# Performance work log

Hardware: AMD Instinct MI355X
Metric: run time of the kernel (lower is better)

## Reference

```python
import jax, jax.numpy as jnp
import numpy as np

N_NODES = 100000
N_EDGES = 1600000
N_GRAPHS = 1024
TIME_DIM = 64
HID = 32
HEADS = 4
NEG_SLOPE = 0.2


def _gat_layer(x, src, dst, W, a_src, a_dst, bias, heads, out_dim):
    # PyG GATConv: h = x @ W, per-head attention, segment softmax over incoming edges at dst.
    N = x.shape[0]
    h = (x @ W).reshape(N, heads, out_dim)                     # [N, H, D]
    alpha_src = jnp.sum(h * a_src, axis=-1)                    # [N, H]
    alpha_dst = jnp.sum(h * a_dst, axis=-1)                    # [N, H]
    e = alpha_src[src] + alpha_dst[dst]                        # [E, H]
    e = jnp.where(e > 0, e, NEG_SLOPE * e)                     # LeakyReLU(0.2)
    m = jax.ops.segment_max(e, dst, num_segments=N)            # [N, H]
    m = jnp.where(jnp.isfinite(m), m, 0.0)
    ex = jnp.exp(e - m[dst])                                   # [E, H]
    s = jax.ops.segment_sum(ex, dst, num_segments=N)           # [N, H]
    alpha = ex / (s[dst] + 1e-16)                              # [E, H]
    msg = h[src] * alpha[..., None]                            # [E, H, D]
    out = jax.ops.segment_sum(msg, dst, num_segments=N)        # [N, H, D]
    return out.reshape(N, heads * out_dim) + bias


def setup_inputs() -> dict:
    key = jax.random.key(0)
    ks = jax.random.split(key, 12)
    x = jax.random.normal(ks[0], (N_NODES, TIME_DIM), jnp.float32)
    edge_index = jax.random.randint(ks[1], (2, N_EDGES), 0, N_NODES, jnp.int32)
    batch = jnp.sort(jax.random.randint(ks[2], (N_NODES,), 0, N_GRAPHS, jnp.int32))
    s = 0.1
    params = {
        "W1": jax.random.normal(ks[3], (TIME_DIM, HEADS * HID), jnp.float32) * s,
        "a_src1": jax.random.normal(ks[4], (HEADS, HID), jnp.float32) * s,
        "a_dst1": jax.random.normal(ks[5], (HEADS, HID), jnp.float32) * s,
        "b1": jnp.zeros((HEADS * HID,), jnp.float32),
        "W2": jax.random.normal(ks[6], (HEADS * HID, HID), jnp.float32) * s,
        "a_src2": jax.random.normal(ks[7], (1, HID), jnp.float32) * s,
        "a_dst2": jax.random.normal(ks[8], (1, HID), jnp.float32) * s,
        "b2": jnp.zeros((HID,), jnp.float32),
        "Wc": jax.random.normal(ks[9], (HID, 1), jnp.float32) * s,
        "bc": jnp.zeros((1,), jnp.float32),
    }
    return dict(x=x, edge_index=edge_index, batch=batch, **params)


def reference(x, edge_index, batch, W1, a_src1, a_dst1, b1, W2, a_src2, a_dst2, b2, Wc, bc):
    N = x.shape[0]
    # PyG GATConv adds self-loops by default.
    loops = jnp.arange(N, dtype=edge_index.dtype)
    src = jnp.concatenate([edge_index[0], loops])
    dst = jnp.concatenate([edge_index[1], loops])

    h1 = jax.nn.relu(_gat_layer(x, src, dst, W1, a_src1, a_dst1, b1, HEADS, HID))
    h2 = jax.nn.relu(_gat_layer(h1, src, dst, W2, a_src2, a_dst2, b2, 1, HID))

    # global_mean_pool over batch ids
    sums = jax.ops.segment_sum(h2, batch, num_segments=N_GRAPHS)          # [G, HID]
    cnts = jax.ops.segment_sum(jnp.ones((N,), h2.dtype), batch, num_segments=N_GRAPHS)
    pooled = sums / jnp.maximum(cnts, 1.0)[:, None]

    return jax.nn.sigmoid(pooled @ Wc + bc)                               # [G, 1]
```

## Files before the change

### kernel.cpp

```cpp
#include <hip/hip_runtime.h>
#include <hip/hip_bf16.h>

#define BSH 7
#define MAXNB 800
#define STILE 4096
#define BCAP 4096

#if __has_builtin(__builtin_amdgcn_cvt_scalef32_pk_fp4_f32) && __has_builtin(__builtin_amdgcn_cvt_scalef32_pk_f32_fp4)
#define USE_FP4 1
#else
#define USE_FP4 0
#endif

__device__ inline float bf_lo(unsigned u) { return __uint_as_float(u << 16); }
__device__ inline float bf_hi(unsigned u) { return __uint_as_float(u & 0xffff0000u); }
__device__ inline unsigned bfpack(float x, float y) {
    unsigned lo = (unsigned)__bfloat16_as_ushort(__float2bfloat16(x));
    unsigned hi = ((unsigned)__bfloat16_as_ushort(__float2bfloat16(y))) << 16;
    return lo | hi;
}


__global__ __launch_bounds__(256) void k_bscatter(const int* __restrict__ ei, int E, int NB,
                                                  int* __restrict__ bcur, int* __restrict__ pairs) {
    __shared__ int lh[MAXNB];
    __shared__ int lbase[MAXNB];
    int t = threadIdx.x;
    int e0 = blockIdx.x * STILE;
    int e1 = min(E, e0 + STILE);
    for (int i = t; i < NB; i += 256) lh[i] = 0;
    __syncthreads();
    int myd[16];
    int q = 0;
    for (int e = e0 + t; e < e1; e += 256, q++) {
        int d = ei[E + e];
        myd[q] = d;
        atomicAdd(&lh[d >> BSH], 1);
    }
    __syncthreads();
    for (int i = t; i < NB; i += 256) {
        int c = lh[i];
        lbase[i] = c ? atomicAdd(&bcur[i], c) : 0;
    }
    __syncthreads();
    for (int i = t; i < NB; i += 256) lh[i] = 0;
    __syncthreads();
    q = 0;
    for (int e = e0 + t; e < e1; e += 256, q++) {
        int s = ei[e];
        int d = myd[q];
        int bk = d >> BSH;
        int off = atomicAdd(&lh[bk], 1);
        pairs[(size_t)bk * BCAP + lbase[bk] + off] = (s << BSH) | (d & ((1 << BSH) - 1));
    }
}

__global__ __launch_bounds__(256) void k_build(const int* __restrict__ pairs,
                                               const int* __restrict__ bcur, int N, int NB,
                                               int2* __restrict__ span, int* __restrict__ csr) {
    __shared__ int lcnt[128];
    __shared__ int loff[128];
    __shared__ int lcur[128];
    int b = blockIdx.x, t = threadIdx.x;
    int node0 = b << BSH;
    size_t base = (size_t)b * BCAP;
    int ne = bcur[b];
    if (t < 128) lcnt[t] = 0;
    __syncthreads();
    for (int i = t; i < ne; i += 256) atomicAdd(&lcnt[pairs[base + i] & 127], 1);
    __syncthreads();
    if (t < 128) loff[t] = lcnt[t];
    __syncthreads();
#pragma unroll
    for (int off = 1; off < 128; off <<= 1) {
        int v = (t < 128 && t >= off) ? loff[t - off] : 0;
        __syncthreads();
        if (t < 128) loff[t] += v;
        __syncthreads();
    }
    if (t < 128) {
        int excl = loff[t] - lcnt[t];
        int n = node0 + t;
        if (n < N) span[n] = make_int2((int)base + excl, (int)base + excl + lcnt[t]);
        lcur[t] = excl;
    }
    __syncthreads();
    for (int i = t; i < ne; i += 256) {
        int p = pairs[base + i];
        int pos = (int)base + atomicAdd(&lcur[p & 127], 1);
        csr[pos] = ((unsigned)p) >> BSH;
    }
}


__global__ __launch_bounds__(256) void k_gemm1(const float* __restrict__ x, const float* __restrict__ W1,
                                               const float* __restrict__ asw, const float* __restrict__ adw,
                                               unsigned* __restrict__ h8, float2* __restrict__ aP,
                                               float2* __restrict__ aDp, int N) {
    __shared__ float xt[64][36];
    int t = threadIdx.x;
    int n0 = blockIdx.x * 32;
    for (int i = t; i < 32 * 64; i += 256) {
        int r = i >> 6, k = i & 63;
        xt[k][r] = (n0 + r < N) ? x[(size_t)(n0 + r) * 64 + k] : 0.f;
    }
    __syncthreads();
    int cg = t & 31, rg = t >> 5;
    int c0 = cg * 4, r0 = rg * 4;
    int head = c0 >> 5;
    const float* Wp = W1 + c0;
    float acc[4][4];
#pragma unroll
    for (int r = 0; r < 4; r++)
#pragma unroll
        for (int c = 0; c < 4; c++) acc[r][c] = 0.f;
#pragma unroll 4
    for (int k = 0; k < 64; k++) {
        float4 wv = *(const float4*)(Wp + (size_t)k * 128);
        float4 xv = *(const float4*)&xt[k][r0];
        float xr;
        xr = xv.x; acc[0][0]=fmaf(xr,wv.x,acc[0][0]); acc[0][1]=fmaf(xr,wv.y,acc[0][1]); acc[0][2]=fmaf(xr,wv.z,acc[0][2]); acc[0][3]=fmaf(xr,wv.w,acc[0][3]);
        xr = xv.y; acc[1][0]=fmaf(xr,wv.x,acc[1][0]); acc[1][1]=fmaf(xr,wv.y,acc[1][1]); acc[1][2]=fmaf(xr,wv.z,acc[1][2]); acc[1][3]=fmaf(xr,wv.w,acc[1][3]);
        xr = xv.z; acc[2][0]=fmaf(xr,wv.x,acc[2][0]); acc[2][1]=fmaf(xr,wv.y,acc[2][1]); acc[2][2]=fmaf(xr,wv.z,acc[2][2]); acc[2][3]=fmaf(xr,wv.w,acc[2][3]);
        xr = xv.w; acc[3][0]=fmaf(xr,wv.x,acc[3][0]); acc[3][1]=fmaf(xr,wv.y,acc[3][1]); acc[3][2]=fmaf(xr,wv.z,acc[3][2]); acc[3][3]=fmaf(xr,wv.w,acc[3][3]);
    }
#if USE_FP4
#pragma unroll
    for (int r = 0; r < 4; r++) {
        int n = n0 + r0 + r;
        if (n < N) {
            unsigned u = __builtin_amdgcn_cvt_scalef32_pk_fp4_f32(0u, acc[r][0], acc[r][1], 1.0f, 0);
            u = __builtin_amdgcn_cvt_scalef32_pk_fp4_f32(u, acc[r][2], acc[r][3], 1.0f, 1);
            ((unsigned short*)h8)[(size_t)n * 32 + (c0 >> 2)] = (unsigned short)(u & 0xffffu);
        }
    }
#else
#pragma unroll
    for (int r = 0; r < 4; r++) {
        int n = n0 + r0 + r;
        if (n < N) {
            int u = __builtin_amdgcn_cvt_pk_fp8_f32(acc[r][0], acc[r][1], 0, false);
            u = __builtin_amdgcn_cvt_pk_fp8_f32(acc[r][2], acc[r][3], u, true);
            h8[(size_t)n * 32 + (c0 >> 2)] = (unsigned)u;
        }
    }
#endif
    float4 awv = *(const float4*)(asw + c0);
    float4 dwv = *(const float4*)(adw + c0);
#pragma unroll
    for (int r = 0; r < 4; r++) {
        float as = acc[r][0] * awv.x + acc[r][1] * awv.y + acc[r][2] * awv.z + acc[r][3] * awv.w;
        float ad = acc[r][0] * dwv.x + acc[r][1] * dwv.y + acc[r][2] * dwv.z + acc[r][3] * dwv.w;
#pragma unroll
        for (int m = 1; m < 8; m <<= 1) { as += __shfl_xor(as, m); ad += __shfl_xor(ad, m); }
        int n = n0 + r0 + r;
        if ((t & 7) == 0 && n < N) {
            aP[n * 4 + head]  = make_float2(__expf(as), __expf(0.2f * as));
            aDp[n * 4 + head] = make_float2(__expf(ad), __expf(0.2f * ad));
        }
    }
}


#if USE_FP4
__device__ inline void fp4fma(unsigned u, float w, float* a) {
    auto f0 = __builtin_amdgcn_cvt_scalef32_pk_f32_fp4(u, 1.0f, 0);
    auto f1 = __builtin_amdgcn_cvt_scalef32_pk_f32_fp4(u, 1.0f, 1);
    auto f2 = __builtin_amdgcn_cvt_scalef32_pk_f32_fp4(u, 1.0f, 2);
    auto f3 = __builtin_amdgcn_cvt_scalef32_pk_f32_fp4(u, 1.0f, 3);
    a[0] = fmaf(w, f0[0], a[0]); a[1] = fmaf(w, f0[1], a[1]);
    a[2] = fmaf(w, f1[0], a[2]); a[3] = fmaf(w, f1[1], a[3]);
    a[4] = fmaf(w, f2[0], a[4]); a[5] = fmaf(w, f2[1], a[5]);
    a[6] = fmaf(w, f3[0], a[6]); a[7] = fmaf(w, f3[1], a[7]);
}

__global__ __launch_bounds__(256) void k_gat1(const unsigned* __restrict__ h4,
                                              const float2* __restrict__ aP, const float2* __restrict__ aDp,
                                              const int2* __restrict__ span, const int* __restrict__ csr,
                                              const float* __restrict__ b1, unsigned* __restrict__ out, int N) {
    int t = threadIdx.x;
    int n = blockIdx.x * 4 + (t >> 6);
    if (n >= N) return;
    int lane = t & 63;
    int e4 = lane >> 4, c = lane & 15;
    int head = c >> 2;
    float2 dnp = aDp[n * 4 + head];
    float ec = dnp.x, ed = dnp.y;
    float2 psf = aP[n * 4 + head];
    float w_self = fmaxf(psf.x * ec, psf.y * ed);
    int2 sp = span[n];
    int beg = sp.x, end = sp.y;

    float a[8] = {0, 0, 0, 0, 0, 0, 0, 0};
    float s = 0.f;
    if (e4 == 0) {
        unsigned u = h4[(size_t)n * 16 + c];
        fp4fma(u, w_self, a);
        s = w_self;
    }
    int j = beg + e4;
    for (; j + 4 < end; j += 8) {
        int s0 = csr[j], s1 = csr[j + 4];
        float2 p0 = aP[s0 * 4 + head], p1 = aP[s1 * 4 + head];
        unsigned u0 = h4[(size_t)s0 * 16 + c];
        unsigned u1 = h4[(size_t)s1 * 16 + c];
        float w0 = fmaxf(p0.x * ec, p0.y * ed);
        float w1 = fmaxf(p1.x * ec, p1.y * ed);
        s += w0 + w1;
        fp4fma(u0, w0, a);
        fp4fma(u1, w1, a);
    }
    for (; j < end; j += 4) {
        int sj = csr[j];
        float2 p = aP[sj * 4 + head];
        unsigned u = h4[(size_t)sj * 16 + c];
        float w = fmaxf(p.x * ec, p.y * ed);
        s += w;
        fp4fma(u, w, a);
    }
#pragma unroll
    for (int off = 16; off < 64; off <<= 1) {
#pragma unroll
        for (int i = 0; i < 8; i++) a[i] += __shfl_xor(a[i], off);
        s += __shfl_xor(s, off);
    }
    if (e4 == 0) {
        float inv = 1.f / (s + 1e-16f);
        float4 ba = ((const float4*)b1)[c * 2];
        float4 bb = ((const float4*)b1)[c * 2 + 1];
        float o0 = fmaxf(fmaf(a[0], inv, ba.x), 0.f);
        float o1 = fmaxf(fmaf(a[1], inv, ba.y), 0.f);
        float o2 = fmaxf(fmaf(a[2], inv, ba.z), 0.f);
        float o3 = fmaxf(fmaf(a[3], inv, ba.w), 0.f);
        float o4 = fmaxf(fmaf(a[4], inv, bb.x), 0.f);
        float o5 = fmaxf(fmaf(a[5], inv, bb.y), 0.f);
        float o6 = fmaxf(fmaf(a[6], inv, bb.z), 0.f);
        float o7 = fmaxf(fmaf(a[7], inv, bb.w), 0.f);
        uint4 o;
        o.x = bfpack(o0, o1); o.y = bfpack(o2, o3);
        o.z = bfpack(o4, o5); o.w = bfpack(o6, o7);
        ((uint4*)out)[(size_t)n * 16 + c] = o;
    }
}
#else
__global__ __launch_bounds__(256) void k_gat1(const unsigned* __restrict__ h8,
                                              const float2* __restrict__ aP, const float2* __restrict__ aDp,
                                              const int2* __restrict__ span, const int* __restrict__ csr,
                                              const float* __restrict__ b1, unsigned* __restrict__ out, int N) {
    int t = threadIdx.x;
    int n = blockIdx.x * 4 + (t >> 6);
    if (n >= N) return;
    int lane = t & 63;
    int e2 = lane >> 5, c = lane & 31;
    int head = c >> 3;
    float2 dnp = aDp[n * 4 + head];
    float ec = dnp.x, ed = dnp.y;
    float2 psf = aP[n * 4 + head];
    float w_self = fmaxf(psf.x * ec, psf.y * ed);
    int2 sp = span[n];
    int beg = sp.x, end = sp.y;

    float a0 = 0.f, a1 = 0.f, a2 = 0.f, a3 = 0.f, s = 0.f;
    if (e2 == 0) {
        unsigned u = h8[(size_t)n * 32 + c];
        auto f01 = __builtin_amdgcn_cvt_pk_f32_fp8((int)u, false);
        auto f23 = __builtin_amdgcn_cvt_pk_f32_fp8((int)u, true);
        a0 = w_self * f01[0]; a1 = w_self * f01[1];
        a2 = w_self * f23[0]; a3 = w_self * f23[1];
        s = w_self;
    }
    int j = beg + e2;
    for (; j + 6 < end; j += 8) {
        int s0 = csr[j], s1 = csr[j + 2], s2 = csr[j + 4], s3 = csr[j + 6];
        float2 p0 = aP[s0 * 4 + head];
        float2 p1 = aP[s1 * 4 + head];
        float2 p2 = aP[s2 * 4 + head];
        float2 p3 = aP[s3 * 4 + head];
        unsigned u0 = h8[(size_t)s0 * 32 + c];
        unsigned u1 = h8[(size_t)s1 * 32 + c];
        unsigned u2 = h8[(size_t)s2 * 32 + c];
        unsigned u3 = h8[(size_t)s3 * 32 + c];
        float w0 = fmaxf(p0.x * ec, p0.y * ed);
        float w1 = fmaxf(p1.x * ec, p1.y * ed);
        float w2 = fmaxf(p2.x * ec, p2.y * ed);
        float w3 = fmaxf(p3.x * ec, p3.y * ed);
        s += w0 + w1 + w2 + w3;
        { auto f01 = __builtin_amdgcn_cvt_pk_f32_fp8((int)u0, false); auto f23 = __builtin_amdgcn_cvt_pk_f32_fp8((int)u0, true);
          a0 = fmaf(w0, f01[0], a0); a1 = fmaf(w0, f01[1], a1); a2 = fmaf(w0, f23[0], a2); a3 = fmaf(w0, f23[1], a3); }
        { auto f01 = __builtin_amdgcn_cvt_pk_f32_fp8((int)u1, false); auto f23 = __builtin_amdgcn_cvt_pk_f32_fp8((int)u1, true);
          a0 = fmaf(w1, f01[0], a0); a1 = fmaf(w1, f01[1], a1); a2 = fmaf(w1, f23[0], a2); a3 = fmaf(w1, f23[1], a3); }
        { auto f01 = __builtin_amdgcn_cvt_pk_f32_fp8((int)u2, false); auto f23 = __builtin_amdgcn_cvt_pk_f32_fp8((int)u2, true);
          a0 = fmaf(w2, f01[0], a0); a1 = fmaf(w2, f01[1], a1); a2 = fmaf(w2, f23[0], a2); a3 = fmaf(w2, f23[1], a3); }
        { auto f01 = __builtin_amdgcn_cvt_pk_f32_fp8((int)u3, false); auto f23 = __builtin_amdgcn_cvt_pk_f32_fp8((int)u3, true);
          a0 = fmaf(w3, f01[0], a0); a1 = fmaf(w3, f01[1], a1); a2 = fmaf(w3, f23[0], a2); a3 = fmaf(w3, f23[1], a3); }
    }
    for (; j < end; j += 2) {
        int sj = csr[j];
        float2 p = aP[sj * 4 + head];
        unsigned u = h8[(size_t)sj * 32 + c];
        float w = fmaxf(p.x * ec, p.y * ed);
        s += w;
        auto f01 = __builtin_amdgcn_cvt_pk_f32_fp8((int)u, false);
        auto f23 = __builtin_amdgcn_cvt_pk_f32_fp8((int)u, true);
        a0 = fmaf(w, f01[0], a0); a1 = fmaf(w, f01[1], a1);
        a2 = fmaf(w, f23[0], a2); a3 = fmaf(w, f23[1], a3);
    }
    a0 += __shfl_xor(a0, 32); a1 += __shfl_xor(a1, 32);
    a2 += __shfl_xor(a2, 32); a3 += __shfl_xor(a3, 32);
    s  += __shfl_xor(s, 32);
    if (e2 == 0) {
        float inv = 1.f / (s + 1e-16f);
        float4 b = ((const float4*)b1)[c];
        float o0 = fmaxf(fmaf(a0, inv, b.x), 0.f);
        float o1 = fmaxf(fmaf(a1, inv, b.y), 0.f);
        float o2 = fmaxf(fmaf(a2, inv, b.z), 0.f);
        float o3 = fmaxf(fmaf(a3, inv, b.w), 0.f);
        ((uint2*)out)[(size_t)n * 32 + c] = make_uint2(bfpack(o0, o1), bfpack(o2, o3));
    }
}
#endif


__global__ __launch_bounds__(256) void k_gemm2(const unsigned* __restrict__ h1b, const float* __restrict__ W2,
                                               const float* __restrict__ asw, const float* __restrict__ adw,
                                               unsigned short* __restrict__ h8, float2* __restrict__ aP,
                                               float2* __restrict__ aDp, int N) {
    __shared__ float xt[128][36];
    int t = threadIdx.x;
    int n0 = blockIdx.x * 32;
    for (int i = t; i < 32 * 64; i += 256) {
        int r = i >> 6, c = i & 63;
        unsigned u = (n0 + r < N) ? h1b[(size_t)(n0 + r) * 64 + c] : 0u;
        xt[2 * c][r]     = bf_lo(u);
        xt[2 * c + 1][r] = bf_hi(u);
    }
    __syncthreads();
    int col = t & 31, grp = t >> 5;
    const float* Wc = W2 + col;
    float acc[4] = {0, 0, 0, 0};
#pragma unroll 4
    for (int k = 0; k < 128; k++) {
        float w = Wc[k * 32];
        float4 xv = *(const float4*)&xt[k][grp * 4];
        acc[0] = fmaf(xv.x, w, acc[0]); acc[1] = fmaf(xv.y, w, acc[1]);
        acc[2] = fmaf(xv.z, w, acc[2]); acc[3] = fmaf(xv.w, w, acc[3]);
    }
    float aw = asw[col], dw = adw[col];
#pragma unroll
    for (int i = 0; i < 4; i++) {
        int n = n0 + grp * 4 + i;
        float other = __shfl_xor(acc[i], 1);
        if (((col & 1) == 0) && n < N) {
            int pk = __builtin_amdgcn_cvt_pk_fp8_f32(acc[i], other, 0, false);
            h8[(size_t)n * 16 + (col >> 1)] = (unsigned short)pk;
        }
        float as = acc[i] * aw, ad = acc[i] * dw;
#pragma unroll
        for (int mm = 16; mm >= 1; mm >>= 1) { as += __shfl_xor(as, mm); ad += __shfl_xor(ad, mm); }
        if (col == 0 && n < N) {
            aP[n]  = make_float2(__expf(as), __expf(0.2f * as));
            aDp[n] = make_float2(__expf(ad), __expf(0.2f * ad));
        }
    }
}


__global__ __launch_bounds__(256) void k_gat2(const unsigned* __restrict__ h8,
                                              const float2* __restrict__ aP, const float2* __restrict__ aDp,
                                              const int2* __restrict__ span, const int* __restrict__ csr,
                                              const float* __restrict__ b2, float* __restrict__ out, int N) {
    int t = threadIdx.x;
    int n = blockIdx.x * 4 + (t >> 6);
    if (n >= N) return;
    int lane = t & 63;
    int e8 = lane >> 3, c = lane & 7;
    float2 dnp = aDp[n];
    float ec = dnp.x, ed = dnp.y;
    float2 psf = aP[n];
    float w_self = fmaxf(psf.x * ec, psf.y * ed);
    int2 sp = span[n];
    int beg = sp.x, end = sp.y;

    float a0 = 0.f, a1 = 0.f, a2 = 0.f, a3 = 0.f, s = 0.f;
    if (e8 == 0) {
        unsigned u = h8[(size_t)n * 8 + c];
        auto f01 = __builtin_amdgcn_cvt_pk_f32_fp8((int)u, false);
        auto f23 = __builtin_amdgcn_cvt_pk_f32_fp8((int)u, true);
        a0 = w_self * f01[0]; a1 = w_self * f01[1];
        a2 = w_self * f23[0]; a3 = w_self * f23[1];
        s = w_self;
    }
    int j = beg + e8;
    for (; j + 24 < end; j += 32) {
        int s0 = csr[j], s1 = csr[j + 8], s2 = csr[j + 16], s3 = csr[j + 24];
        float2 p0 = aP[s0], p1 = aP[s1], p2 = aP[s2], p3 = aP[s3];
        unsigned u0 = h8[(size_t)s0 * 8 + c];
        unsigned u1 = h8[(size_t)s1 * 8 + c];
        unsigned u2 = h8[(size_t)s2 * 8 + c];
        unsigned u3 = h8[(size_t)s3 * 8 + c];
        float w0 = fmaxf(p0.x * ec, p0.y * ed);
        float w1 = fmaxf(p1.x * ec, p1.y * ed);
        float w2 = fmaxf(p2.x * ec, p2.y * ed);
        float w3 = fmaxf(p3.x * ec, p3.y * ed);
        s += w0 + w1 + w2 + w3;
        { auto f01 = __builtin_amdgcn_cvt_pk_f32_fp8((int)u0, false); auto f23 = __builtin_amdgcn_cvt_pk_f32_fp8((int)u0, true);
          a0 = fmaf(w0, f01[0], a0); a1 = fmaf(w0, f01[1], a1); a2 = fmaf(w0, f23[0], a2); a3 = fmaf(w0, f23[1], a3); }
        { auto f01 = __builtin_amdgcn_cvt_pk_f32_fp8((int)u1, false); auto f23 = __builtin_amdgcn_cvt_pk_f32_fp8((int)u1, true);
          a0 = fmaf(w1, f01[0], a0); a1 = fmaf(w1, f01[1], a1); a2 = fmaf(w1, f23[0], a2); a3 = fmaf(w1, f23[1], a3); }
        { auto f01 = __builtin_amdgcn_cvt_pk_f32_fp8((int)u2, false); auto f23 = __builtin_amdgcn_cvt_pk_f32_fp8((int)u2, true);
          a0 = fmaf(w2, f01[0], a0); a1 = fmaf(w2, f01[1], a1); a2 = fmaf(w2, f23[0], a2); a3 = fmaf(w2, f23[1], a3); }
        { auto f01 = __builtin_amdgcn_cvt_pk_f32_fp8((int)u3, false); auto f23 = __builtin_amdgcn_cvt_pk_f32_fp8((int)u3, true);
          a0 = fmaf(w3, f01[0], a0); a1 = fmaf(w3, f01[1], a1); a2 = fmaf(w3, f23[0], a2); a3 = fmaf(w3, f23[1], a3); }
    }
    for (; j < end; j += 8) {
        int sj = csr[j];
        float2 p = aP[sj];
        unsigned u = h8[(size_t)sj * 8 + c];
        float w = fmaxf(p.x * ec, p.y * ed);
        s += w;
        auto f01 = __builtin_amdgcn_cvt_pk_f32_fp8((int)u, false);
        auto f23 = __builtin_amdgcn_cvt_pk_f32_fp8((int)u, true);
        a0 = fmaf(w, f01[0], a0); a1 = fmaf(w, f01[1], a1);
        a2 = fmaf(w, f23[0], a2); a3 = fmaf(w, f23[1], a3);
    }
#pragma unroll
    for (int off = 8; off < 64; off <<= 1) {
        a0 += __shfl_xor(a0, off); a1 += __shfl_xor(a1, off);
        a2 += __shfl_xor(a2, off); a3 += __shfl_xor(a3, off);
        s  += __shfl_xor(s, off);
    }
    if (e8 == 0) {
        float inv = 1.f / (s + 1e-16f);
        float4 b = ((const float4*)b2)[c];
        float4 o;
        o.x = fmaxf(fmaf(a0, inv, b.x), 0.f);
        o.y = fmaxf(fmaf(a1, inv, b.y), 0.f);
        o.z = fmaxf(fmaf(a2, inv, b.z), 0.f);
        o.w = fmaxf(fmaf(a3, inv, b.w), 0.f);
        ((float4*)out)[(size_t)n * 8 + c] = o;
    }
}


__global__ void k_pool(const float* __restrict__ h2r, const int* __restrict__ batch, int N,
                       const float* __restrict__ Wc, const float* __restrict__ bc,
                       float* __restrict__ out) {
    int g = blockIdx.x;
    int t = threadIdx.x, d = t & 31, r = t >> 5;
    int lo = 0, hi = N;
    while (lo < hi) { int mid = (lo + hi) >> 1; if (batch[mid] < g) lo = mid + 1; else hi = mid; }
    int start = lo;
    hi = N;
    while (lo < hi) { int mid = (lo + hi) >> 1; if (batch[mid] < g + 1) lo = mid + 1; else hi = mid; }
    int end = lo;
    float sum = 0.f;
    for (int i = start + r; i < end; i += 2) sum += h2r[(size_t)i * 32 + d];
    sum += __shfl_xor(sum, 32);
    float cnt = (float)(end - start);
    float mean = sum / fmaxf(cnt, 1.f);
    float v = mean * Wc[d];
#pragma unroll
    for (int m = 16; m >= 1; m >>= 1) v += __shfl_xor(v, m);
    if (t == 0) out[g] = 1.f / (1.f + expf(-(v + bc[0])));
}


extern "C" void kernel_launch(void* const* d_in, const int* in_sizes, int n_in,
                              void* d_out, int out_size, void* d_ws, size_t ws_size,
                              hipStream_t stream) {
    const float* x    = (const float*)d_in[0];
    const int*   ei   = (const int*)d_in[1];
    const int*   batch= (const int*)d_in[2];
    const float* W1   = (const float*)d_in[3];
    const float* as1  = (const float*)d_in[4];
    const float* ad1  = (const float*)d_in[5];
    const float* b1   = (const float*)d_in[6];
    const float* W2   = (const float*)d_in[7];
    const float* as2  = (const float*)d_in[8];
    const float* ad2  = (const float*)d_in[9];
    const float* b2   = (const float*)d_in[10];
    const float* Wc   = (const float*)d_in[11];
    const float* bc   = (const float*)d_in[12];

    const int N = in_sizes[0] / 64;
    const int E = in_sizes[1] / 2;
    const int G = out_size;
    const int NB = (N + 127) >> BSH;

    size_t off = 0;
    char* base = (char*)d_ws;
    auto alloc = [&](size_t bytes) -> char* {
        char* p = base + off;
        off += (bytes + 255) & ~(size_t)255;
        return p;
    };
    int*      bcur  = (int*)alloc((size_t)NB * 4);
    int*      pairs = (int*)alloc((size_t)NB * BCAP * 4);
    int2*     span  = (int2*)alloc((size_t)N * 8);
    int*      csr   = (int*)alloc((size_t)NB * BCAP * 4);
    unsigned* h8_1  = (unsigned*)alloc((size_t)N * 128);
    unsigned* h1b   = (unsigned*)alloc((size_t)N * 64 * 4);
    float2*   aP1   = (float2*)alloc((size_t)N * 4 * 8);
    float2*   aDp1  = (float2*)alloc((size_t)N * 4 * 8);
    unsigned short* h8_2 = (unsigned short*)alloc((size_t)N * 32);
    float*    h2r   = (float*)alloc((size_t)N * 32 * 4);
    float2*   aP2   = (float2*)alloc((size_t)N * 8);
    float2*   aDp2  = (float2*)alloc((size_t)N * 8);
    (void)ws_size; (void)n_in;

    hipMemsetAsync(bcur, 0, (size_t)NB * 4, stream);
    k_bscatter<<<(E + STILE - 1) / STILE, 256, 0, stream>>>(ei, E, NB, bcur, pairs);
    k_build<<<NB, 256, 0, stream>>>(pairs, bcur, N, NB, span, csr);

    k_gemm1<<<(N + 31) / 32, 256, 0, stream>>>(x, W1, as1, ad1, h8_1, aP1, aDp1, N);
    k_gat1<<<(N + 3) / 4, 256, 0, stream>>>(h8_1, aP1, aDp1, span, csr, b1, h1b, N);

    k_gemm2<<<(N + 31) / 32, 256, 0, stream>>>(h1b, W2, as2, ad2, h8_2, aP2, aDp2, N);
    k_gat2<<<(N + 3) / 4, 256, 0, stream>>>((const unsigned*)h8_2, aP2, aDp2, span, csr, b2, h2r, N);

    k_pool<<<G, 64, 0, stream>>>(h2r, batch, N, Wc, bc, (float*)d_out);
}
```

Before: 237.2 us.

## Fuse scatter with gemm1, pack attention coefs to bf16, fp4 layer2, atomic pooling

Merges the edge bucket-scatter and the first projection GEMM into one launch, with blocks split by index, and removes the fp8 fallback path. The per-node source attention exponentials are packed as bf16 pairs instead of float2, which halves gather traffic in both GAT layers. Layer-2 features are stored as fp4, and the GAT2 epilogue atomically accumulates into per-graph pooled sums. This removes the h2 round trip and the pool reduction, but adds float-atomic contention and extra quantization error.

```diff
diff --git a/kernel.cpp b/kernel.cpp
--- a/kernel.cpp
+++ b/kernel.cpp
@@ -5,12 +5,6 @@
 #define MAXNB 800
 #define STILE 4096
 #define BCAP 4096
-
-#if __has_builtin(__builtin_amdgcn_cvt_scalef32_pk_fp4_f32) && __has_builtin(__builtin_amdgcn_cvt_scalef32_pk_f32_fp4)
-#define USE_FP4 1
-#else
-#define USE_FP4 0
-#endif
 
 __device__ inline float bf_lo(unsigned u) { return __uint_as_float(u << 16); }
 __device__ inline float bf_hi(unsigned u) { return __uint_as_float(u & 0xffff0000u); }
@@ -20,40 +14,109 @@
     return lo | hi;
 }
 
-
-__global__ __launch_bounds__(256) void k_bscatter(const int* __restrict__ ei, int E, int NB,
-                                                  int* __restrict__ bcur, int* __restrict__ pairs) {
-    __shared__ int lh[MAXNB];
-    __shared__ int lbase[MAXNB];
+__device__ inline void fp4fma(unsigned u, float w, float* a) {
+    auto f0 = __builtin_amdgcn_cvt_scalef32_pk_f32_fp4(u, 1.0f, 0);
+    auto f1 = __builtin_amdgcn_cvt_scalef32_pk_f32_fp4(u, 1.0f, 1);
+    auto f2 = __builtin_amdgcn_cvt_scalef32_pk_f32_fp4(u, 1.0f, 2);
+    auto f3 = __builtin_amdgcn_cvt_scalef32_pk_f32_fp4(u, 1.0f, 3);
+    a[0] = fmaf(w, f0[0], a[0]); a[1] = fmaf(w, f0[1], a[1]);
+    a[2] = fmaf(w, f1[0], a[2]); a[3] = fmaf(w, f1[1], a[3]);
+    a[4] = fmaf(w, f2[0], a[4]); a[5] = fmaf(w, f2[1], a[5]);
+    a[6] = fmaf(w, f3[0], a[6]); a[7] = fmaf(w, f3[1], a[7]);
+}
+
+
+__global__ __launch_bounds__(256) void k_front(const int* __restrict__ ei, int E, int NB,
+                                               int* __restrict__ bcur, int* __restrict__ pairs,
+                                               const float* __restrict__ x, const float* __restrict__ W1,
+                                               const float* __restrict__ asw, const float* __restrict__ adw,
+                                               unsigned* __restrict__ h4, unsigned* __restrict__ aPq,
+                                               float2* __restrict__ aDp, int N, int nbsc) {
+    __shared__ union USm {
+        struct { int lh[MAXNB]; int lbase[MAXNB]; } sc;
+        float xt[64][36];
+    } sm;
     int t = threadIdx.x;
-    int e0 = blockIdx.x * STILE;
-    int e1 = min(E, e0 + STILE);
-    for (int i = t; i < NB; i += 256) lh[i] = 0;
-    __syncthreads();
-    int myd[16];
-    int q = 0;
-    for (int e = e0 + t; e < e1; e += 256, q++) {
-        int d = ei[E + e];
-        myd[q] = d;
-        atomicAdd(&lh[d >> BSH], 1);
-    }
-    __syncthreads();
-    for (int i = t; i < NB; i += 256) {
-        int c = lh[i];
-        lbase[i] = c ? atomicAdd(&bcur[i], c) : 0;
-    }
-    __syncthreads();
-    for (int i = t; i < NB; i += 256) lh[i] = 0;
-    __syncthreads();
-    q = 0;
-    for (int e = e0 + t; e < e1; e += 256, q++) {
-        int s = ei[e];
-        int d = myd[q];
-        int bk = d >> BSH;
-        int off = atomicAdd(&lh[bk], 1);
-        pairs[(size_t)bk * BCAP + lbase[bk] + off] = (s << BSH) | (d & ((1 << BSH) - 1));
-    }
-}
+    if (blockIdx.x < nbsc) {
+        int e0 = blockIdx.x * STILE;
+        int e1 = min(E, e0 + STILE);
+        for (int i = t; i < NB; i += 256) sm.sc.lh[i] = 0;
+        __syncthreads();
+        int myd[16];
+        int q = 0;
+        for (int e = e0 + t; e < e1; e += 256, q++) {
+            int d = ei[E + e];
+            myd[q] = d;
+            atomicAdd(&sm.sc.lh[d >> BSH], 1);
+        }
+        __syncthreads();
+        for (int i = t; i < NB; i += 256) {
+            int c = sm.sc.lh[i];
+            sm.sc.lbase[i] = c ? atomicAdd(&bcur[i], c) : 0;
+        }
+        __syncthreads();
+        for (int i = t; i < NB; i += 256) sm.sc.lh[i] = 0;
+        __syncthreads();
+        q = 0;
+        for (int e = e0 + t; e < e1; e += 256, q++) {
+            int s = ei[e];
+            int d = myd[q];
+            int bk = d >> BSH;
+            int off = atomicAdd(&sm.sc.lh[bk], 1);
+            pairs[(size_t)bk * BCAP + sm.sc.lbase[bk] + off] = (s << BSH) | (d & ((1 << BSH) - 1));
+        }
+        return;
+    }
+    int n0 = (blockIdx.x - nbsc) * 32;
+    for (int i = t; i < 32 * 64; i += 256) {
+        int r = i >> 6, k = i & 63;
+        sm.xt[k][r] = (n0 + r < N) ? x[(size_t)(n0 + r) * 64 + k] : 0.f;
+    }
+    __syncthreads();
+    int cg = t & 31, rg = t >> 5;
+    int c0 = cg * 4, r0 = rg * 4;
+    int head = c0 >> 5;
+    const float* Wp = W1 + c0;
+    float acc[4][4];
+#pragma unroll
+    for (int r = 0; r < 4; r++)
+#pragma unroll
+        for (int c = 0; c < 4; c++) acc[r][c] = 0.f;
+#pragma unroll 4
+    for (int k = 0; k < 64; k++) {
+        float4 wv = *(const float4*)(Wp + (size_t)k * 128);
+        float4 xv = *(const float4*)&sm.xt[k][r0];
+        float xr;
+        xr = xv.x; acc[0][0]=fmaf(xr,wv.x,acc[0][0]); acc[0][1]=fmaf(xr,wv.y,acc[0][1]); acc[0][2]=fmaf(xr,wv.z,acc[0][2]); acc[0][3]=fmaf(xr,wv.w,acc[0][3]);
+        xr = xv.y; acc[1][0]=fmaf(xr,wv.x,acc[1][0]); acc[1][1]=fmaf(xr,wv.y,acc[1][1]); acc[1][2]=fmaf(xr,wv.z,acc[1][2]); acc[1][3]=fmaf(xr,wv.w,acc[1][3]);
+        xr = xv.z; acc[2][0]=fmaf(xr,wv.x,acc[2][0]); acc[2][1]=fmaf(xr,wv.y,acc[2][1]); acc[2][2]=fmaf(xr,wv.z,acc[2][2]); acc[2][3]=fmaf(xr,wv.w,acc[2][3]);
+        xr = xv.w; acc[3][0]=fmaf(xr,wv.x,acc[3][0]); acc[3][1]=fmaf(xr,wv.y,acc[3][1]); acc[3][2]=fmaf(xr,wv.z,acc[3][2]); acc[3][3]=fmaf(xr,wv.w,acc[3][3]);
+    }
+#pragma unroll
+    for (int r = 0; r < 4; r++) {
+        int n = n0 + r0 + r;
+        if (n < N) {
+            unsigned u = __builtin_amdgcn_cvt_scalef32_pk_fp4_f32(0u, acc[r][0], acc[r][1], 1.0f, 0);
+            u = __builtin_amdgcn_cvt_scalef32_pk_fp4_f32(u, acc[r][2], acc[r][3], 1.0f, 1);
+            ((unsigned short*)h4)[(size_t)n * 32 + cg] = (unsigned short)(u & 0xffffu);
+        }
+    }
+    float4 awv = *(const float4*)(asw + c0);
+    float4 dwv = *(const float4*)(adw + c0);
+#pragma unroll
+    for (int r = 0; r < 4; r++) {
+        float as = acc[r][0] * awv.x + acc[r][1] * awv.y + acc[r][2] * awv.z + acc[r][3] * awv.w;
+        float ad = acc[r][0] * dwv.x + acc[r][1] * dwv.y + acc[r][2] * dwv.z + acc[r][3] * dwv.w;
+#pragma unroll
+        for (int m = 1; m < 8; m <<= 1) { as += __shfl_xor(as, m); ad += __shfl_xor(ad, m); }
+        int n = n0 + r0 + r;
+        if ((t & 7) == 0 && n < N) {
+            aPq[n * 4 + head] = bfpack(__expf(as), __expf(0.2f * as));
+            aDp[n * 4 + head] = make_float2(__expf(ad), __expf(0.2f * ad));
+        }
+    }
+}
+
 
 __global__ __launch_bounds__(256) void k_build(const int* __restrict__ pairs,
                                                const int* __restrict__ bcur, int N, int NB,
@@ -93,89 +156,8 @@
 }
 
 
-__global__ __launch_bounds__(256) void k_gemm1(const float* __restrict__ x, const float* __restrict__ W1,
-                                               const float* __restrict__ asw, const float* __restrict__ adw,
-                                               unsigned* __restrict__ h8, float2* __restrict__ aP,
-                                               float2* __restrict__ aDp, int N) {
-    __shared__ float xt[64][36];
-    int t = threadIdx.x;
-    int n0 = blockIdx.x * 32;
-    for (int i = t; i < 32 * 64; i += 256) {
-        int r = i >> 6, k = i & 63;
-        xt[k][r] = (n0 + r < N) ? x[(size_t)(n0 + r) * 64 + k] : 0.f;
-    }
-    __syncthreads();
-    int cg = t & 31, rg = t >> 5;
-    int c0 = cg * 4, r0 = rg * 4;
-    int head = c0 >> 5;
-    const float* Wp = W1 + c0;
-    float acc[4][4];
-#pragma unroll
-    for (int r = 0; r < 4; r++)
-#pragma unroll
-        for (int c = 0; c < 4; c++) acc[r][c] = 0.f;
-#pragma unroll 4
-    for (int k = 0; k < 64; k++) {
-        float4 wv = *(const float4*)(Wp + (size_t)k * 128);
-        float4 xv = *(const float4*)&xt[k][r0];
-        float xr;
-        xr = xv.x; acc[0][0]=fmaf(xr,wv.x,acc[0][0]); acc[0][1]=fmaf(xr,wv.y,acc[0][1]); acc[0][2]=fmaf(xr,wv.z,acc[0][2]); acc[0][3]=fmaf(xr,wv.w,acc[0][3]);
-        xr = xv.y; acc[1][0]=fmaf(xr,wv.x,acc[1][0]); acc[1][1]=fmaf(xr,wv.y,acc[1][1]); acc[1][2]=fmaf(xr,wv.z,acc[1][2]); acc[1][3]=fmaf(xr,wv.w,acc[1][3]);
-        xr = xv.z; acc[2][0]=fmaf(xr,wv.x,acc[2][0]); acc[2][1]=fmaf(xr,wv.y,acc[2][1]); acc[2][2]=fmaf(xr,wv.z,acc[2][2]); acc[2][3]=fmaf(xr,wv.w,acc[2][3]);
-        xr = xv.w; acc[3][0]=fmaf(xr,wv.x,acc[3][0]); acc[3][1]=fmaf(xr,wv.y,acc[3][1]); acc[3][2]=fmaf(xr,wv.z,acc[3][2]); acc[3][3]=fmaf(xr,wv.w,acc[3][3]);
-    }
-#if USE_FP4
-#pragma unroll
-    for (int r = 0; r < 4; r++) {
-        int n = n0 + r0 + r;
-        if (n < N) {
-            unsigned u = __builtin_amdgcn_cvt_scalef32_pk_fp4_f32(0u, acc[r][0], acc[r][1], 1.0f, 0);
-            u = __builtin_amdgcn_cvt_scalef32_pk_fp4_f32(u, acc[r][2], acc[r][3], 1.0f, 1);
-            ((unsigned short*)h8)[(size_t)n * 32 + (c0 >> 2)] = (unsigned short)(u & 0xffffu);
-        }
-    }
-#else
-#pragma unroll
-    for (int r = 0; r < 4; r++) {
-        int n = n0 + r0 + r;
-        if (n < N) {
-            int u = __builtin_amdgcn_cvt_pk_fp8_f32(acc[r][0], acc[r][1], 0, false);
-            u = __builtin_amdgcn_cvt_pk_fp8_f32(acc[r][2], acc[r][3], u, true);
-            h8[(size_t)n * 32 + (c0 >> 2)] = (unsigned)u;
-        }
-    }
-#endif
-    float4 awv = *(const float4*)(asw + c0);
-    float4 dwv = *(const float4*)(adw + c0);
-#pragma unroll
-    for (int r = 0; r < 4; r++) {
-        float as = acc[r][0] * awv.x + acc[r][1] * awv.y + acc[r][2] * awv.z + acc[r][3] * awv.w;
-        float ad = acc[r][0] * dwv.x + acc[r][1] * dwv.y + acc[r][2] * dwv.z + acc[r][3] * dwv.w;
-#pragma unroll
-        for (int m = 1; m < 8; m <<= 1) { as += __shfl_xor(as, m); ad += __shfl_xor(ad, m); }
-        int n = n0 + r0 + r;
-        if ((t & 7) == 0 && n < N) {
-            aP[n * 4 + head]  = make_float2(__expf(as), __expf(0.2f * as));
-            aDp[n * 4 + head] = make_float2(__expf(ad), __expf(0.2f * ad));
-        }
-    }
-}
-
-
-#if USE_FP4
-__device__ inline void fp4fma(unsigned u, float w, float* a) {
-    auto f0 = __builtin_amdgcn_cvt_scalef32_pk_f32_fp4(u, 1.0f, 0);
-    auto f1 = __builtin_amdgcn_cvt_scalef32_pk_f32_fp4(u, 1.0f, 1);
-    auto f2 = __builtin_amdgcn_cvt_scalef32_pk_f32_fp4(u, 1.0f, 2);
-    auto f3 = __builtin_amdgcn_cvt_scalef32_pk_f32_fp4(u, 1.0f, 3);
-    a[0] = fmaf(w, f0[0], a[0]); a[1] = fmaf(w, f0[1], a[1]);
-    a[2] = fmaf(w, f1[0], a[2]); a[3] = fmaf(w, f1[1], a[3]);
-    a[4] = fmaf(w, f2[0], a[4]); a[5] = fmaf(w, f2[1], a[5]);
-    a[6] = fmaf(w, f3[0], a[6]); a[7] = fmaf(w, f3[1], a[7]);
-}
-
 __global__ __launch_bounds__(256) void k_gat1(const unsigned* __restrict__ h4,
-                                              const float2* __restrict__ aP, const float2* __restrict__ aDp,
+                                              const unsigned* __restrict__ aPq, const float2* __restrict__ aDp,
                                               const int2* __restrict__ span, const int* __restrict__ csr,
                                               const float* __restrict__ b1, unsigned* __restrict__ out, int N) {
     int t = threadIdx.x;
@@ -186,35 +168,34 @@
     int head = c >> 2;
     float2 dnp = aDp[n * 4 + head];
     float ec = dnp.x, ed = dnp.y;
-    float2 psf = aP[n * 4 + head];
-    float w_self = fmaxf(psf.x * ec, psf.y * ed);
+    unsigned apn = aPq[n * 4 + head];
+    float w_self = fmaxf(bf_lo(apn) * ec, bf_hi(apn) * ed);
     int2 sp = span[n];
     int beg = sp.x, end = sp.y;
 
     float a[8] = {0, 0, 0, 0, 0, 0, 0, 0};
     float s = 0.f;
     if (e4 == 0) {
-        unsigned u = h4[(size_t)n * 16 + c];
-        fp4fma(u, w_self, a);
+        fp4fma(h4[(size_t)n * 16 + c], w_self, a);
         s = w_self;
     }
     int j = beg + e4;
     for (; j + 4 < end; j += 8) {
         int s0 = csr[j], s1 = csr[j + 4];
-        float2 p0 = aP[s0 * 4 + head], p1 = aP[s1 * 4 + head];
+        unsigned ap0 = aPq[s0 * 4 + head], ap1 = aPq[s1 * 4 + head];
         unsigned u0 = h4[(size_t)s0 * 16 + c];
         unsigned u1 = h4[(size_t)s1 * 16 + c];
-        float w0 = fmaxf(p0.x * ec, p0.y * ed);
-        float w1 = fmaxf(p1.x * ec, p1.y * ed);
+        float w0 = fmaxf(bf_lo(ap0) * ec, bf_hi(ap0) * ed);
+        float w1 = fmaxf(bf_lo(ap1) * ec, bf_hi(ap1) * ed);
         s += w0 + w1;
         fp4fma(u0, w0, a);
         fp4fma(u1, w1, a);
     }
     for (; j < end; j += 4) {
         int sj = csr[j];
-        float2 p = aP[sj * 4 + head];
+        unsigned ap = aPq[sj * 4 + head];
         unsigned u = h4[(size_t)sj * 16 + c];
-        float w = fmaxf(p.x * ec, p.y * ed);
+        float w = fmaxf(bf_lo(ap) * ec, bf_hi(ap) * ed);
         s += w;
         fp4fma(u, w, a);
     }
@@ -242,88 +223,11 @@
         ((uint4*)out)[(size_t)n * 16 + c] = o;
     }
 }
-#else
-__global__ __launch_bounds__(256) void k_gat1(const unsigned* __restrict__ h8,
-                                              const float2* __restrict__ aP, const float2* __restrict__ aDp,
-                                              const int2* __restrict__ span, const int* __restrict__ csr,
-                                              const float* __restrict__ b1, unsigned* __restrict__ out, int N) {
-    int t = threadIdx.x;
-    int n = blockIdx.x * 4 + (t >> 6);
-    if (n >= N) return;
-    int lane = t & 63;
-    int e2 = lane >> 5, c = lane & 31;
-    int head = c >> 3;
-    float2 dnp = aDp[n * 4 + head];
-    float ec = dnp.x, ed = dnp.y;
-    float2 psf = aP[n * 4 + head];
-    float w_self = fmaxf(psf.x * ec, psf.y * ed);
-    int2 sp = span[n];
-    int beg = sp.x, end = sp.y;
-
-    float a0 = 0.f, a1 = 0.f, a2 = 0.f, a3 = 0.f, s = 0.f;
-    if (e2 == 0) {
-        unsigned u = h8[(size_t)n * 32 + c];
-        auto f01 = __builtin_amdgcn_cvt_pk_f32_fp8((int)u, false);
-        auto f23 = __builtin_amdgcn_cvt_pk_f32_fp8((int)u, true);
-        a0 = w_self * f01[0]; a1 = w_self * f01[1];
-        a2 = w_self * f23[0]; a3 = w_self * f23[1];
-        s = w_self;
-    }
-    int j = beg + e2;
-    for (; j + 6 < end; j += 8) {
-        int s0 = csr[j], s1 = csr[j + 2], s2 = csr[j + 4], s3 = csr[j + 6];
-        float2 p0 = aP[s0 * 4 + head];
-        float2 p1 = aP[s1 * 4 + head];
-        float2 p2 = aP[s2 * 4 + head];
-        float2 p3 = aP[s3 * 4 + head];
-        unsigned u0 = h8[(size_t)s0 * 32 + c];
-        unsigned u1 = h8[(size_t)s1 * 32 + c];
-        unsigned u2 = h8[(size_t)s2 * 32 + c];
-        unsigned u3 = h8[(size_t)s3 * 32 + c];
-        float w0 = fmaxf(p0.x * ec, p0.y * ed);
-        float w1 = fmaxf(p1.x * ec, p1.y * ed);
-        float w2 = fmaxf(p2.x * ec, p2.y * ed);
-        float w3 = fmaxf(p3.x * ec, p3.y * ed);
-        s += w0 + w1 + w2 + w3;
-        { auto f01 = __builtin_amdgcn_cvt_pk_f32_fp8((int)u0, false); auto f23 = __builtin_amdgcn_cvt_pk_f32_fp8((int)u0, true);
-          a0 = fmaf(w0, f01[0], a0); a1 = fmaf(w0, f01[1], a1); a2 = fmaf(w0, f23[0], a2); a3 = fmaf(w0, f23[1], a3); }
-        { auto f01 = __builtin_amdgcn_cvt_pk_f32_fp8((int)u1, false); auto f23 = __builtin_amdgcn_cvt_pk_f32_fp8((int)u1, true);
-          a0 = fmaf(w1, f01[0], a0); a1 = fmaf(w1, f01[1], a1); a2 = fmaf(w1, f23[0], a2); a3 = fmaf(w1, f23[1], a3); }
-        { auto f01 = __builtin_amdgcn_cvt_pk_f32_fp8((int)u2, false); auto f23 = __builtin_amdgcn_cvt_pk_f32_fp8((int)u2, true);
-          a0 = fmaf(w2, f01[0], a0); a1 = fmaf(w2, f01[1], a1); a2 = fmaf(w2, f23[0], a2); a3 = fmaf(w2, f23[1], a3); }
-        { auto f01 = __builtin_amdgcn_cvt_pk_f32_fp8((int)u3, false); auto f23 = __builtin_amdgcn_cvt_pk_f32_fp8((int)u3, true);
-          a0 = fmaf(w3, f01[0], a0); a1 = fmaf(w3, f01[1], a1); a2 = fmaf(w3, f23[0], a2); a3 = fmaf(w3, f23[1], a3); }
-    }
-    for (; j < end; j += 2) {
-        int sj = csr[j];
-        float2 p = aP[sj * 4 + head];
-        unsigned u = h8[(size_t)sj * 32 + c];
-        float w = fmaxf(p.x * ec, p.y * ed);
-        s += w;
-        auto f01 = __builtin_amdgcn_cvt_pk_f32_fp8((int)u, false);
-        auto f23 = __builtin_amdgcn_cvt_pk_f32_fp8((int)u, true);
-        a0 = fmaf(w, f01[0], a0); a1 = fmaf(w, f01[1], a1);
-        a2 = fmaf(w, f23[0], a2); a3 = fmaf(w, f23[1], a3);
-    }
-    a0 += __shfl_xor(a0, 32); a1 += __shfl_xor(a1, 32);
-    a2 += __shfl_xor(a2, 32); a3 += __shfl_xor(a3, 32);
-    s  += __shfl_xor(s, 32);
-    if (e2 == 0) {
-        float inv = 1.f / (s + 1e-16f);
-        float4 b = ((const float4*)b1)[c];
-        float o0 = fmaxf(fmaf(a0, inv, b.x), 0.f);
-        float o1 = fmaxf(fmaf(a1, inv, b.y), 0.f);
-        float o2 = fmaxf(fmaf(a2, inv, b.z), 0.f);
-        float o3 = fmaxf(fmaf(a3, inv, b.w), 0.f);
-        ((uint2*)out)[(size_t)n * 32 + c] = make_uint2(bfpack(o0, o1), bfpack(o2, o3));
-    }
-}
-#endif
 
 
 __global__ __launch_bounds__(256) void k_gemm2(const unsigned* __restrict__ h1b, const float* __restrict__ W2,
                                                const float* __restrict__ asw, const float* __restrict__ adw,
-                                               unsigned short* __restrict__ h8, float2* __restrict__ aP,
+                                               unsigned short* __restrict__ h4b, unsigned* __restrict__ aPq,
                                                float2* __restrict__ aDp, int N) {
     __shared__ float xt[128][36];
     int t = threadIdx.x;
@@ -335,130 +239,119 @@
         xt[2 * c + 1][r] = bf_hi(u);
     }
     __syncthreads();
-    int col = t & 31, grp = t >> 5;
-    const float* Wc = W2 + col;
-    float acc[4] = {0, 0, 0, 0};
+    int cg = t & 7, rg = t >> 3;
+    int c0 = cg * 4;
+    const float* Wp = W2 + c0;
+    float a0 = 0.f, a1 = 0.f, a2 = 0.f, a3 = 0.f;
 #pragma unroll 4
     for (int k = 0; k < 128; k++) {
-        float w = Wc[k * 32];
-        float4 xv = *(const float4*)&xt[k][grp * 4];
-        acc[0] = fmaf(xv.x, w, acc[0]); acc[1] = fmaf(xv.y, w, acc[1]);
-        acc[2] = fmaf(xv.z, w, acc[2]); acc[3] = fmaf(xv.w, w, acc[3]);
-    }
-    float aw = asw[col], dw = adw[col];
-#pragma unroll
-    for (int i = 0; i < 4; i++) {
-        int n = n0 + grp * 4 + i;
-        float other = __shfl_xor(acc[i], 1);
-        if (((col & 1) == 0) && n < N) {
-            int pk = __builtin_amdgcn_cvt_pk_fp8_f32(acc[i], other, 0, false);
-            h8[(size_t)n * 16 + (col >> 1)] = (unsigned short)pk;
-        }
-        float as = acc[i] * aw, ad = acc[i] * dw;
-#pragma unroll
-        for (int mm = 16; mm >= 1; mm >>= 1) { as += __shfl_xor(as, mm); ad += __shfl_xor(ad, mm); }
-        if (col == 0 && n < N) {
-            aP[n]  = make_float2(__expf(as), __expf(0.2f * as));
-            aDp[n] = make_float2(__expf(ad), __expf(0.2f * ad));
-        }
-    }
-}
-
-
-__global__ __launch_bounds__(256) void k_gat2(const unsigned* __restrict__ h8,
-                                              const float2* __restrict__ aP, const float2* __restrict__ aDp,
+        float4 wv = *(const float4*)(Wp + (size_t)k * 32);
+        float xr = xt[k][rg];
+        a0 = fmaf(xr, wv.x, a0); a1 = fmaf(xr, wv.y, a1);
+        a2 = fmaf(xr, wv.z, a2); a3 = fmaf(xr, wv.w, a3);
+    }
+    int n = n0 + rg;
+    if (n < N) {
+        unsigned u = __builtin_amdgcn_cvt_scalef32_pk_fp4_f32(0u, a0, a1, 1.0f, 0);
+        u = __builtin_amdgcn_cvt_scalef32_pk_fp4_f32(u, a2, a3, 1.0f, 1);
+        h4b[(size_t)n * 8 + cg] = (unsigned short)(u & 0xffffu);
+    }
+    float4 awv = *(const float4*)(asw + c0);
+    float4 dwv = *(const float4*)(adw + c0);
+    float as = a0 * awv.x + a1 * awv.y + a2 * awv.z + a3 * awv.w;
+    float ad = a0 * dwv.x + a1 * dwv.y + a2 * dwv.z + a3 * dwv.w;
+#pragma unroll
+    for (int m = 1; m < 8; m <<= 1) { as += __shfl_xor(as, m); ad += __shfl_xor(ad, m); }
+    if (cg == 0 && n < N) {
+        aPq[n] = bfpack(__expf(as), __expf(0.2f * as));
+        aDp[n] = make_float2(__expf(ad), __expf(0.2f * ad));
+    }
+}
+
+
+__global__ __launch_bounds__(256) void k_gat2(const unsigned* __restrict__ h4,
+                                              const unsigned* __restrict__ aPq, const float2* __restrict__ aDp,
                                               const int2* __restrict__ span, const int* __restrict__ csr,
-                                              const float* __restrict__ b2, float* __restrict__ out, int N) {
+                                              const float* __restrict__ b2, const int* __restrict__ batch,
+                                              float* __restrict__ pooled, int N) {
     int t = threadIdx.x;
     int n = blockIdx.x * 4 + (t >> 6);
     if (n >= N) return;
     int lane = t & 63;
-    int e8 = lane >> 3, c = lane & 7;
+    int e16 = lane >> 2, c = lane & 3;
     float2 dnp = aDp[n];
     float ec = dnp.x, ed = dnp.y;
-    float2 psf = aP[n];
-    float w_self = fmaxf(psf.x * ec, psf.y * ed);
+    unsigned apn = aPq[n];
+    float w_self = fmaxf(bf_lo(apn) * ec, bf_hi(apn) * ed);
     int2 sp = span[n];
     int beg = sp.x, end = sp.y;
 
-    float a0 = 0.f, a1 = 0.f, a2 = 0.f, a3 = 0.f, s = 0.f;
-    if (e8 == 0) {
-        unsigned u = h8[(size_t)n * 8 + c];
-        auto f01 = __builtin_amdgcn_cvt_pk_f32_fp8((int)u, false);
-        auto f23 = __builtin_amdgcn_cvt_pk_f32_fp8((int)u, true);
-        a0 = w_self * f01[0]; a1 = w_self * f01[1];
-        a2 = w_self * f23[0]; a3 = w_self * f23[1];
+    float a[8] = {0, 0, 0, 0, 0, 0, 0, 0};
+    float s = 0.f;
+    if (e16 == 0) {
+        fp4fma(h4[(size_t)n * 4 + c], w_self, a);
         s = w_self;
     }
-    int j = beg + e8;
-    for (; j + 24 < end; j += 32) {
-        int s0 = csr[j], s1 = csr[j + 8], s2 = csr[j + 16], s3 = csr[j + 24];
-        float2 p0 = aP[s0], p1 = aP[s1], p2 = aP[s2], p3 = aP[s3];
-        unsigned u0 = h8[(size_t)s0 * 8 + c];
-        unsigned u1 = h8[(size_t)s1 * 8 + c];
-        unsigned u2 = h8[(size_t)s2 * 8 + c];
-        unsigned u3 = h8[(size_t)s3 * 8 + c];
-        float w0 = fmaxf(p0.x * ec, p0.y * ed);
-        float w1 = fmaxf(p1.x * ec, p1.y * ed);
-        float w2 = fmaxf(p2.x * ec, p2.y * ed);
-        float w3 = fmaxf(p3.x * ec, p3.y * ed);
-        s += w0 + w1 + w2 + w3;
-        { auto f01 = __builtin_amdgcn_cvt_pk_f32_fp8((int)u0, false); auto f23 = __builtin_amdgcn_cvt_pk_f32_fp8((int)u0, true);
-          a0 = fmaf(w0, f01[0], a0); a1 = fmaf(w0, f01[1], a1); a2 = fmaf(w0, f23[0], a2); a3 = fmaf(w0, f23[1], a3); }
-        { auto f01 = __builtin_amdgcn_cvt_pk_f32_fp8((int)u1, false); auto f23 = __builtin_amdgcn_cvt_pk_f32_fp8((int)u1, true);
-          a0 = fmaf(w1, f01[0], a0); a1 = fmaf(w1, f01[1], a1); a2 = fmaf(w1, f23[0], a2); a3 = fmaf(w1, f23[1], a3); }
-        { auto f01 = __builtin_amdgcn_cvt_pk_f32_fp8((int)u2, false); auto f23 = __builtin_amdgcn_cvt_pk_f32_fp8((int)u2, true);
-          a0 = fmaf(w2, f01[0], a0); a1 = fmaf(w2, f01[1], a1); a2 = fmaf(w2, f23[0], a2); a3 = fmaf(w2, f23[1], a3); }
-        { auto f01 = __builtin_amdgcn_cvt_pk_f32_fp8((int)u3, false); auto f23 = __builtin_amdgcn_cvt_pk_f32_fp8((int)u3, true);
-          a0 = fmaf(w3, f01[0], a0); a1 = fmaf(w3, f01[1], a1); a2 = fmaf(w3, f23[0], a2); a3 = fmaf(w3, f23[1], a3); }
-    }
-    for (; j < end; j += 8) {
+    int j = beg + e16;
+    for (; j + 16 < end; j += 32) {
+        int s0 = csr[j], s1 = csr[j + 16];
+        unsigned ap0 = aPq[s0], ap1 = aPq[s1];
+        unsigned u0 = h4[(size_t)s0 * 4 + c];
+        unsigned u1 = h4[(size_t)s1 * 4 + c];
+        float w0 = fmaxf(bf_lo(ap0) * ec, bf_hi(ap0) * ed);
+        float w1 = fmaxf(bf_lo(ap1) * ec, bf_hi(ap1) * ed);
+        s += w0 + w1;
+        fp4fma(u0, w0, a);
+        fp4fma(u1, w1, a);
+    }
+    for (; j < end; j += 16) {
         int sj = csr[j];
-        float2 p = aP[sj];
-        unsigned u = h8[(size_t)sj * 8 + c];
-        float w = fmaxf(p.x * ec, p.y * ed);
+        unsigned ap = aPq[sj];
+        unsigned u = h4[(size_t)sj * 4 + c];
+        float w = fmaxf(bf_lo(ap) * ec, bf_hi(ap) * ed);
         s += w;
-        auto f01 = __builtin_amdgcn_cvt_pk_f32_fp8((int)u, false);
-        auto f23 = __builtin_amdgcn_cvt_pk_f32_fp8((int)u, true);
-        a0 = fmaf(w, f01[0], a0); a1 = fmaf(w, f01[1], a1);
-        a2 = fmaf(w, f23[0], a2); a3 = fmaf(w, f23[1], a3);
-    }
-#pragma unroll
-    for (int off = 8; off < 64; off <<= 1) {
-        a0 += __shfl_xor(a0, off); a1 += __shfl_xor(a1, off);
-        a2 += __shfl_xor(a2, off); a3 += __shfl_xor(a3, off);
-        s  += __shfl_xor(s, off);
-    }
-    if (e8 == 0) {
+        fp4fma(u, w, a);
+    }
+#pragma unroll
+    for (int off = 4; off < 64; off <<= 1) {
+#pragma unroll
+        for (int i = 0; i < 8; i++) a[i] += __shfl_xor(a[i], off);
+        s += __shfl_xor(s, off);
+    }
+    if (e16 == 0) {
         float inv = 1.f / (s + 1e-16f);
-        float4 b = ((const float4*)b2)[c];
-        float4 o;
-        o.x = fmaxf(fmaf(a0, inv, b.x), 0.f);
-        o.y = fmaxf(fmaf(a1, inv, b.y), 0.f);
-        o.z = fmaxf(fmaf(a2, inv, b.z), 0.f);
-        o.w = fmaxf(fmaf(a3, inv, b.w), 0.f);
-        ((float4*)out)[(size_t)n * 8 + c] = o;
-    }
-}
-
-
-__global__ void k_pool(const float* __restrict__ h2r, const int* __restrict__ batch, int N,
-                       const float* __restrict__ Wc, const float* __restrict__ bc,
-                       float* __restrict__ out) {
+        int g = batch[n];
+        float4 ba = ((const float4*)b2)[c * 2];
+        float4 bb = ((const float4*)b2)[c * 2 + 1];
+        float o0 = fmaxf(fmaf(a[0], inv, ba.x), 0.f);
+        float o1 = fmaxf(fmaf(a[1], inv, ba.y), 0.f);
+        float o2 = fmaxf(fmaf(a[2], inv, ba.z), 0.f);
+        float o3 = fmaxf(fmaf(a[3], inv, ba.w), 0.f);
+        float o4 = fmaxf(fmaf(a[4], inv, bb.x), 0.f);
+        float o5 = fmaxf(fmaf(a[5], inv, bb.y), 0.f);
+        float o6 = fmaxf(fmaf(a[6], inv, bb.z), 0.f);
+        float o7 = fmaxf(fmaf(a[7], inv, bb.w), 0.f);
+        float* pg = pooled + (size_t)g * 32 + c * 8;
+        atomicAdd(pg + 0, o0); atomicAdd(pg + 1, o1);
+        atomicAdd(pg + 2, o2); atomicAdd(pg + 3, o3);
+        atomicAdd(pg + 4, o4); atomicAdd(pg + 5, o5);
+        atomicAdd(pg + 6, o6); atomicAdd(pg + 7, o7);
+    }
+}
+
+
+__global__ void k_cls(const float* __restrict__ pooled, const int* __restrict__ batch, int N,
+                      const float* __restrict__ Wc, const float* __restrict__ bc,
+                      float* __restrict__ out) {
     int g = blockIdx.x;
-    int t = threadIdx.x, d = t & 31, r = t >> 5;
+    int t = threadIdx.x, d = t & 31;
     int lo = 0, hi = N;
     while (lo < hi) { int mid = (lo + hi) >> 1; if (batch[mid] < g) lo = mid + 1; else hi = mid; }
     int start = lo;
     hi = N;
     while (lo < hi) { int mid = (lo + hi) >> 1; if (batch[mid] < g + 1) lo = mid + 1; else hi = mid; }
-    int end = lo;
-    float sum = 0.f;
-    for (int i = start + r; i < end; i += 2) sum += h2r[(size_t)i * 32 + d];
-    sum += __shfl_xor(sum, 32);
-    float cnt = (float)(end - start);
-    float mean = sum / fmaxf(cnt, 1.f);
-    float v = mean * Wc[d];
+    float cnt = (float)(lo - start);
+    float v = pooled[(size_t)g * 32 + d] / fmaxf(cnt, 1.f) * Wc[d];
 #pragma unroll
     for (int m = 16; m >= 1; m >>= 1) v += __shfl_xor(v, m);
     if (t == 0) out[g] = 1.f / (1.f + expf(-(v + bc[0])));
@@ -498,25 +391,30 @@
     int*      pairs = (int*)alloc((size_t)NB * BCAP * 4);
     int2*     span  = (int2*)alloc((size_t)N * 8);
     int*      csr   = (int*)alloc((size_t)NB * BCAP * 4);
-    unsigned* h8_1  = (unsigned*)alloc((size_t)N * 128);
+    unsigned* h4_1  = (unsigned*)alloc((size_t)N * 64);
     unsigned* h1b   = (unsigned*)alloc((size_t)N * 64 * 4);
-    float2*   aP1   = (float2*)alloc((size_t)N * 4 * 8);
+    unsigned* aPq1  = (unsigned*)alloc((size_t)N * 4 * 4);
     float2*   aDp1  = (float2*)alloc((size_t)N * 4 * 8);
-    unsigned short* h8_2 = (unsigned short*)alloc((size_t)N * 32);
-    float*    h2r   = (float*)alloc((size_t)N * 32 * 4);
-    float2*   aP2   = (float2*)alloc((size_t)N * 8);
+    unsigned short* h4_2 = (unsigned short*)alloc((size_t)N * 16);
+    unsigned* aPq2  = (unsigned*)alloc((size_t)N * 4);
     float2*   aDp2  = (float2*)alloc((size_t)N * 8);
+    float*    pooled= (float*)alloc((size_t)G * 32 * 4);
     (void)ws_size; (void)n_in;
 
+    const int nbsc = (E + STILE - 1) / STILE;
+
     hipMemsetAsync(bcur, 0, (size_t)NB * 4, stream);
-    k_bscatter<<<(E + STILE - 1) / STILE, 256, 0, stream>>>(ei, E, NB, bcur, pairs);
+    hipMemsetAsync(pooled, 0, (size_t)G * 32 * 4, stream);
+
+    k_front<<<nbsc + (N + 31) / 32, 256, 0, stream>>>(ei, E, NB, bcur, pairs,
+                                                      x, W1, as1, ad1, h4_1, aPq1, aDp1, N, nbsc);
     k_build<<<NB, 256, 0, stream>>>(pairs, bcur, N, NB, span, csr);
 
-    k_gemm1<<<(N + 31) / 32, 256, 0, stream>>>(x, W1, as1, ad1, h8_1, aP1, aDp1, N);
-    k_gat1<<<(N + 3) / 4, 256, 0, stream>>>(h8_1, aP1, aDp1, span, csr, b1, h1b, N);
-
-    k_gemm2<<<(N + 31) / 32, 256, 0, stream>>>(h1b, W2, as2, ad2, h8_2, aP2, aDp2, N);
-    k_gat2<<<(N + 3) / 4, 256, 0, stream>>>((const unsigned*)h8_2, aP2, aDp2, span, csr, b2, h2r, N);
-
-    k_pool<<<G, 64, 0, stream>>>(h2r, batch, N, Wc, bc, (float*)d_out);
-}
+    k_gat1<<<(N + 3) / 4, 256, 0, stream>>>(h4_1, aPq1, aDp1, span, csr, b1, h1b, N);
+
+    k_gemm2<<<(N + 31) / 32, 256, 0, stream>>>(h1b, W2, as2, ad2, h4_2, aPq2, aDp2, N);
+    k_gat2<<<(N + 3) / 4, 256, 0, stream>>>((const unsigned*)h4_2, aPq2, aDp2, span, csr, b2,
+                                            batch, pooled, N);
+
+    k_cls<<<G, 64, 0, stream>>>(pooled, batch, N, Wc, bc, (float*)d_out);
+}
```

Measured after the change: 348.0 us. 46.7% more time.
